# Performance work log

Hardware: AMD Instinct MI355X
Metric: run time of the kernel (lower is better)

The kernel has to match this reference:

```python
import jax, jax.numpy as jnp
import numpy as np

N_NODES = 100000
N_EDGES = 1600000
DIM = 128
EPS = 1e-12


def l2_normalize(x):
    # F.normalize(x, p=2, dim=1) with eps=1e-12
    n = jnp.linalg.norm(x, axis=1, keepdims=True)
    return x / jnp.maximum(n, EPS)


def poincare_logmap0(x):
    # logmap at origin, curvature c=1: artanh(||x||) * x / ||x||
    n = jnp.linalg.norm(x, axis=1, keepdims=True)
    n_safe = jnp.maximum(n, EPS)
    n_cl = jnp.clip(n_safe, EPS, 1.0 - 1e-5)
    return jnp.arctanh(n_cl) * x / n_safe


def poincare_expmap0(v):
    # expmap at origin, curvature c=1: tanh(||v||) * v / ||v||
    n = jnp.linalg.norm(v, axis=1, keepdims=True)
    n_safe = jnp.maximum(n, EPS)
    return jnp.tanh(n_safe) * v / n_safe


def mean_aggregate(x, src, dst, n_nodes):
    # DGL copy_u + mean: for each dst node, mean of src-node features over
    # incoming edges; nodes with zero in-degree get zeros.
    msg_sum = jax.ops.segment_sum(x[src], dst, num_segments=n_nodes)  # [N, D]
    deg = jax.ops.segment_sum(jnp.ones_like(dst, dtype=x.dtype), dst,
                              num_segments=n_nodes)  # [N]
    deg = deg[:, None]
    return jnp.where(deg > 0, msg_sum / jnp.maximum(deg, 1.0), 0.0)


def setup_inputs() -> dict:
    key = jax.random.key(0)
    ks = jax.random.split(key, 11)
    e_emb = jax.random.normal(ks[0], (N_NODES, DIM), dtype=jnp.float32)
    b_raw = jax.random.normal(ks[1], (N_NODES, DIM), dtype=jnp.float32)
    # project into open unit Poincare ball (max norm ~0.9)
    b_norm = jnp.linalg.norm(b_raw, axis=1, keepdims=True)
    b_emb = b_raw * (0.9 * jnp.tanh(b_norm) / jnp.maximum(b_norm, EPS))
    s_emb = jax.random.normal(ks[2], (N_NODES, DIM), dtype=jnp.float32)
    src = jax.random.randint(ks[3], (N_EDGES,), 0, N_NODES, dtype=jnp.int32)
    dst = jax.random.randint(ks[4], (N_EDGES,), 0, N_NODES, dtype=jnp.int32)
    scale = 1.0 / np.sqrt(DIM)
    W_e = jax.random.uniform(ks[5], (DIM, DIM), jnp.float32, -scale, scale)
    b_e = jax.random.uniform(ks[6], (DIM,), jnp.float32, -scale, scale)
    W_b = jax.random.uniform(ks[7], (DIM, DIM), jnp.float32, -scale, scale)
    b_b = jax.random.uniform(ks[8], (DIM,), jnp.float32, -scale, scale)
    W_s = jax.random.uniform(ks[9], (DIM, DIM), jnp.float32, -scale, scale)
    b_s = jax.random.uniform(ks[10], (DIM,), jnp.float32, -scale, scale)
    return {"e_emb": e_emb, "b_emb": b_emb, "s_emb": s_emb,
            "W_e": W_e, "b_e": b_e, "W_b": W_b, "b_b": b_b,
            "W_s": W_s, "b_s": b_s, "src": src, "dst": dst}


def reference(e_emb, b_emb, s_emb, W_e, b_e, W_b, b_b, W_s, b_s, src, dst):
    n = e_emb.shape[0]
    # Euclidean branch: aggregate -> linear -> LeakyReLU(0.2)
    e_neigh = mean_aggregate(e_emb, src, dst, n)
    e_lin = e_neigh @ W_e.T + b_e
    e_out = jnp.where(e_lin >= 0, e_lin, 0.2 * e_lin)
    # Poincare branch: logmap0 -> linear -> aggregate -> expmap0
    b_tan = poincare_logmap0(b_emb)
    b_tr = b_tan @ W_b.T + b_b
    b_neigh = mean_aggregate(b_tr, src, dst, n)
    b_out = poincare_expmap0(b_neigh)
    # Spherical branch: normalize -> linear -> aggregate -> normalize
    s_nrm = l2_normalize(s_emb)
    s_tr = s_nrm @ W_s.T + b_s
    s_neigh = mean_aggregate(s_tr, src, dst, n)
    s_out = l2_normalize(s_neigh)
    return (e_out, b_out, s_out)
```

## Files before the change

### kernel.cpp

```cpp
#include <hip/hip_runtime.h>
#include <math.h>

#define N_NODESC 100000
#define N_EDGESC 1600000
#define DIMC 128
#define EPSV 1e-12f

typedef __attribute__((ext_vector_type(8))) short short8;
typedef __attribute__((ext_vector_type(4))) float f32x4;
typedef __attribute__((ext_vector_type(2))) float f32x2;

__device__ inline unsigned bf16r(float f) {
    unsigned u = __float_as_uint(f);
    return (u + 0x7FFFu + ((u >> 16) & 1u)) >> 16;
}
__device__ inline unsigned pack2(float lo, float hi) {
    return bf16r(lo) | (bf16r(hi) << 16);
}
__device__ inline float unlo(unsigned u) { return __uint_as_float(u << 16); }
__device__ inline float unhi(unsigned u) { return __uint_as_float(u & 0xFFFF0000u); }

__device__ inline void bfsplit(float f, unsigned& h, unsigned& l) {
    h = bf16r(f);
    float fh = __uint_as_float(h << 16);
    l = bf16r(f - fh);
}

__global__ void pretransform_k(const float* __restrict__ e_emb,
                               const float* __restrict__ b_emb,
                               const float* __restrict__ s_emb,
                               const int* __restrict__ dst,
                               unsigned* __restrict__ tab,
                               int* __restrict__ deg) {
    {
        int e = blockIdx.x * 64 + threadIdx.x;
        if (threadIdx.x < 64 && e < N_EDGESC) atomicAdd(&deg[dst[e]], 1);
    }
    int wave = (blockIdx.x * blockDim.x + threadIdx.x) >> 6;
    int lane = threadIdx.x & 63;
    if (wave >= N_NODESC) return;
    f32x2 ev = __builtin_nontemporal_load((const f32x2*)(e_emb + (size_t)wave * DIMC) + lane);
    f32x2 bv = __builtin_nontemporal_load((const f32x2*)(b_emb + (size_t)wave * DIMC) + lane);
    f32x2 sv = __builtin_nontemporal_load((const f32x2*)(s_emb + (size_t)wave * DIMC) + lane);
    float bss = bv.x * bv.x + bv.y * bv.y;
    float sss = sv.x * sv.x + sv.y * sv.y;
    #pragma unroll
    for (int m = 1; m < 64; m <<= 1) {
        bss += __shfl_xor(bss, m, 64);
        sss += __shfl_xor(sss, m, 64);
    }
    float bn  = sqrtf(bss);
    float bns = fmaxf(bn, EPSV);
    float bcl = fminf(fmaxf(bns, EPSV), 1.0f - 1e-5f);
    float bsc = atanhf(bcl) / bns;
    float sn  = sqrtf(sss);
    float ssc = 1.0f / fmaxf(sn, EPSV);
    unsigned* p = tab + (size_t)wave * 192 + lane * 3;
    uint3 v;
    v.x = pack2(ev.x, ev.y);
    v.y = pack2(bv.x * bsc, bv.y * bsc);
    v.z = pack2(sv.x * ssc, sv.y * ssc);
    *(uint3*)p = v;
}

__global__ void scan1_k(const int* __restrict__ deg, int* __restrict__ scanned,
                        int* __restrict__ partials) {
    __shared__ int s[256];
    int t = threadIdx.x;
    int g = blockIdx.x * 256 + t;
    int v = (g < N_NODESC) ? deg[g] : 0;
    s[t] = v;
    __syncthreads();
    for (int off = 1; off < 256; off <<= 1) {
        int x = (t >= off) ? s[t - off] : 0;
        __syncthreads();
        s[t] += x;
        __syncthreads();
    }
    if (g < N_NODESC) scanned[g] = s[t];
    if (t == 255) partials[blockIdx.x] = s[255];
}

__global__ void scan2_k(const int* __restrict__ partials, int* __restrict__ blockoff, int nb) {
    __shared__ int s[512];
    int t = threadIdx.x;
    int v = (t < nb) ? partials[t] : 0;
    s[t] = v;
    __syncthreads();
    for (int off = 1; off < 512; off <<= 1) {
        int x = (t >= off) ? s[t - off] : 0;
        __syncthreads();
        s[t] += x;
        __syncthreads();
    }
    if (t < nb) blockoff[t] = s[t] - v;
}

__global__ void scan3_k(const int* __restrict__ scanned, const int* __restrict__ blockoff,
                        int* __restrict__ offs) {
    int g = blockIdx.x * 256 + threadIdx.x;
    if (g < N_NODESC) offs[g + 1] = scanned[g] + blockoff[blockIdx.x];
    if (g == 0) offs[0] = 0;
}

__global__ void fill_k(const int* __restrict__ src, const int* __restrict__ dst,
                       const int* __restrict__ offs, int* __restrict__ cursor,
                       int* __restrict__ esrc) {
    int e = blockIdx.x * 256 + threadIdx.x;
    if (e < N_EDGESC) {
        int d = __builtin_nontemporal_load(dst + e);
        int sv = __builtin_nontemporal_load(src + e);
        int pos = offs[d] + atomicAdd(&cursor[d], 1);
        esrc[pos] = sv;
    }
}

__global__ void aggregate_k(const unsigned* __restrict__ tab,
                            const int* __restrict__ offs,
                            const int* __restrict__ esrc,
                            float* __restrict__ out) {
    int wave = (blockIdx.x * blockDim.x + threadIdx.x) >> 6;
    int lane = threadIdx.x & 63;
    if (wave >= N_NODESC) return;
    int beg = offs[wave], end = offs[wave + 1];
    float ae0 = 0.f, ae1 = 0.f, ab0 = 0.f, ab1 = 0.f, as0 = 0.f, as1 = 0.f;
    int j = beg;
    int lo3 = lane * 3;
    for (; j + 1 < end; j += 2) {
        int s0 = esrc[j], s1 = esrc[j + 1];
        uint3 v0 = *(const uint3*)(tab + (size_t)s0 * 192 + lo3);
        uint3 v1 = *(const uint3*)(tab + (size_t)s1 * 192 + lo3);
        ae0 += unlo(v0.x); ae1 += unhi(v0.x);
        ab0 += unlo(v0.y); ab1 += unhi(v0.y);
        as0 += unlo(v0.z); as1 += unhi(v0.z);
        ae0 += unlo(v1.x); ae1 += unhi(v1.x);
        ab0 += unlo(v1.y); ab1 += unhi(v1.y);
        as0 += unlo(v1.z); as1 += unhi(v1.z);
    }
    if (j < end) {
        int s0 = esrc[j];
        uint3 v0 = *(const uint3*)(tab + (size_t)s0 * 192 + lo3);
        ae0 += unlo(v0.x); ae1 += unhi(v0.x);
        ab0 += unlo(v0.y); ab1 += unhi(v0.y);
        as0 += unlo(v0.z); as1 += unhi(v0.z);
    }
    int deg = end - beg;
    float inv = (deg > 0) ? 1.0f / (float)deg : 0.0f;
    ((float2*)(out + (size_t)wave * DIMC))[lane]                           = make_float2(ae0 * inv, ae1 * inv);
    ((float2*)(out + (size_t)(N_NODESC + wave) * DIMC))[lane]              = make_float2(ab0 * inv, ab1 * inv);
    ((float2*)(out + (size_t)(2 * (size_t)N_NODESC + wave) * DIMC))[lane]  = make_float2(as0 * inv, as1 * inv);
}

__global__ __launch_bounds__(256, 2) void gemm_mfma_k(
    float* __restrict__ out,
    const float* __restrict__ W_e, const float* __restrict__ b_e,
    const float* __restrict__ W_b, const float* __restrict__ b_b,
    const float* __restrict__ W_s, const float* __restrict__ b_s,
    const int* __restrict__ deg) {
    __shared__ unsigned short Wh[128][72];
    __shared__ unsigned short Wl[128][72];
    int c = blockIdx.y;
    const float* W    = (c == 0) ? W_e : (c == 1) ? W_b : W_s;
    const float* bias = (c == 0) ? b_e : (c == 1) ? b_b : b_s;
    float* A = out + (size_t)c * N_NODESC * DIMC;

    int tid = threadIdx.x;
    int wid = tid >> 6, lane = tid & 63;
    int m0 = blockIdx.x * 64;
    int arow = m0 + wid * 16 + (lane & 15);
    int kb = (lane >> 4) * 8;
    bool rowok = (arow < N_NODESC);
    const float* Ap = A + (size_t)arow * DIMC + kb;
    int colw = lane & 15;

    f32x4 acc[8] = {};

    for (int h = 0; h < 2; ++h) {
        short8 Ah[2], Al[2];
        #pragma unroll
        for (int ks = 0; ks < 2; ++ks) {
            float4 a0 = make_float4(0.f, 0.f, 0.f, 0.f);
            float4 a1 = a0;
            if (rowok) {
                a0 = *(const float4*)(Ap + h * 64 + ks * 32);
                a1 = *(const float4*)(Ap + h * 64 + ks * 32 + 4);
            }
            #define SPLIT8(val, idx) { unsigned hh, ll; bfsplit(val, hh, ll); \
                Ah[ks][idx] = (short)hh; Al[ks][idx] = (short)ll; }
            SPLIT8(a0.x, 0) SPLIT8(a0.y, 1) SPLIT8(a0.z, 2) SPLIT8(a0.w, 3)
            SPLIT8(a1.x, 4) SPLIT8(a1.y, 5) SPLIT8(a1.z, 6) SPLIT8(a1.w, 7)
            #undef SPLIT8
        }
        if (h) __syncthreads();
        #pragma unroll
        for (int r = 0; r < 8; ++r) {
            int flat = (r * 256 + tid) * 4;
            int n  = flat >> 6;
            int kk = flat & 63;
            float4 w4 = *(const float4*)(W + (size_t)n * DIMC + h * 64 + kk);
            unsigned h0, h1, h2, h3, l0, l1, l2, l3;
            bfsplit(w4.x, h0, l0); bfsplit(w4.y, h1, l1);
            bfsplit(w4.z, h2, l2); bfsplit(w4.w, h3, l3);
            *(uint2*)&Wh[n][kk] = make_uint2(h0 | (h1 << 16), h2 | (h3 << 16));
            *(uint2*)&Wl[n][kk] = make_uint2(l0 | (l1 << 16), l2 | (l3 << 16));
        }
        __syncthreads();
        #pragma unroll
        for (int n = 0; n < 8; ++n) {
            int col = n * 16 + colw;
            #pragma unroll
            for (int ks = 0; ks < 2; ++ks) {
                short8 wh = *(const short8*)&Wh[col][ks * 32 + kb];
                short8 wl = *(const short8*)&Wl[col][ks * 32 + kb];
                acc[n] = __builtin_amdgcn_mfma_f32_16x16x32_bf16(Ah[ks], wh, acc[n], 0, 0, 0);
                acc[n] = __builtin_amdgcn_mfma_f32_16x16x32_bf16(Al[ks], wh, acc[n], 0, 0, 0);
                acc[n] = __builtin_amdgcn_mfma_f32_16x16x32_bf16(Ah[ks], wl, acc[n], 0, 0, 0);
            }
        }
    }

    int r0 = m0 + wid * 16 + (lane >> 4) * 4;
    float bn[8];
    #pragma unroll
    for (int n = 0; n < 8; ++n) bn[n] = bias[n * 16 + colw];

    if (c == 0) {
        #pragma unroll
        for (int rg = 0; rg < 4; ++rg) {
            int row = r0 + rg;
            if (row >= N_NODESC) continue;
            float* Ar = A + (size_t)row * DIMC;
            #pragma unroll
            for (int n = 0; n < 8; ++n) {
                float z = acc[n][rg] + bn[n];
                float o = (z >= 0.f) ? z : 0.2f * z;
                __builtin_nontemporal_store(o, &Ar[n * 16 + colw]);
            }
        }
    } else {
        #pragma unroll
        for (int rg = 0; rg < 4; ++rg) {
            float z[8];
            float ss = 0.f;
            #pragma unroll
            for (int n = 0; n < 8; ++n) {
                z[n] = acc[n][rg] + bn[n];
                ss += z[n] * z[n];
            }
            ss += __shfl_xor(ss, 1, 64);
            ss += __shfl_xor(ss, 2, 64);
            ss += __shfl_xor(ss, 4, 64);
            ss += __shfl_xor(ss, 8, 64);
            float nrm = sqrtf(ss);
            float scale;
            if (c == 1) {
                float nsafe = fmaxf(nrm, EPSV);
                scale = tanhf(nsafe) / nsafe;
            } else {
                scale = 1.0f / fmaxf(nrm, EPSV);
            }
            int row = r0 + rg;
            if (row < N_NODESC) {
                if (deg[row] <= 0) scale = 0.0f;
                float* Ar = A + (size_t)row * DIMC;
                #pragma unroll
                for (int n = 0; n < 8; ++n)
                    __builtin_nontemporal_store(z[n] * scale, &Ar[n * 16 + colw]);
            }
        }
    }
}

extern "C" void kernel_launch(void* const* d_in, const int* in_sizes, int n_in,
                              void* d_out, int out_size, void* d_ws, size_t ws_size,
                              hipStream_t stream) {
    const float* e_emb = (const float*)d_in[0];
    const float* b_emb = (const float*)d_in[1];
    const float* s_emb = (const float*)d_in[2];
    const float* W_e   = (const float*)d_in[3];
    const float* b_e   = (const float*)d_in[4];
    const float* W_b   = (const float*)d_in[5];
    const float* b_b   = (const float*)d_in[6];
    const float* W_s   = (const float*)d_in[7];
    const float* b_s   = (const float*)d_in[8];
    const int*   src   = (const int*)d_in[9];
    const int*   dst   = (const int*)d_in[10];
    float* out = (float*)d_out;

    char* w = (char*)d_ws;
    unsigned* tab = (unsigned*)w; w += (size_t)N_NODESC * 192 * sizeof(unsigned);
    int* deg      = (int*)w;   w += (size_t)N_NODESC * sizeof(int);
    int* cursor   = (int*)w;   w += (size_t)N_NODESC * sizeof(int);
    int* scanned  = (int*)w;   w += (size_t)N_NODESC * sizeof(int);
    int* partials = (int*)w;   w += 512 * sizeof(int);
    int* blockoff = (int*)w;   w += 512 * sizeof(int);
    int* offs     = (int*)w;   w += (size_t)(N_NODESC + 1) * sizeof(int);
    w = (char*)(((uintptr_t)w + 255) & ~(uintptr_t)255);
    int* esrc     = (int*)w;   w += (size_t)N_EDGESC * sizeof(int);

    const int nbScan  = (N_NODESC + 255) / 256;
    const int nbEdge  = (N_EDGESC + 255) / 256;
    const int nbNode4 = (N_NODESC + 3) / 4;
    const int nbTile  = (N_NODESC + 63) / 64;

    hipMemsetAsync(deg, 0, (size_t)2 * N_NODESC * sizeof(int), stream);

    pretransform_k<<<nbNode4, 256, 0, stream>>>(e_emb, b_emb, s_emb, dst, tab, deg);
    scan1_k<<<nbScan, 256, 0, stream>>>(deg, scanned, partials);
    scan2_k<<<1, 512, 0, stream>>>(partials, blockoff, nbScan);
    scan3_k<<<nbScan, 256, 0, stream>>>(scanned, blockoff, offs);
    fill_k<<<nbEdge, 256, 0, stream>>>(src, dst, offs, cursor, esrc);
    aggregate_k<<<nbNode4, 256, 0, stream>>>(tab, offs, esrc, out);
    gemm_mfma_k<<<dim3(nbTile, 3), 256, 0, stream>>>(out, W_e, b_e, W_b, b_b, W_s, b_s, deg);
}
```

Baseline: 632.9 us.

## Split packed feature table into per-channel planes and aggregate each channel separately

The pretransform now writes the three bf16 branch features into three separate planar tables instead of one interleaved 12-byte-per-lane record. The aggregation kernel launches three times as many waves, one per (channel, node), each gathering a compact 256-byte row per edge. The aim is a smaller, contiguous gather footprint per channel and better cache locality. In exchange, the CSR offsets and edge source indices are read three times and each wave issues smaller loads.

```diff
diff --git a/kernel.cpp b/kernel.cpp
--- a/kernel.cpp
+++ b/kernel.cpp
@@ -55,12 +55,10 @@
     float bsc = atanhf(bcl) / bns;
     float sn  = sqrtf(sss);
     float ssc = 1.0f / fmaxf(sn, EPSV);
-    unsigned* p = tab + (size_t)wave * 192 + lane * 3;
-    uint3 v;
-    v.x = pack2(ev.x, ev.y);
-    v.y = pack2(bv.x * bsc, bv.y * bsc);
-    v.z = pack2(sv.x * ssc, sv.y * ssc);
-    *(uint3*)p = v;
+    size_t base = (size_t)wave * 64 + lane;
+    tab[base]                            = pack2(ev.x, ev.y);
+    tab[(size_t)N_NODESC * 64 + base]    = pack2(bv.x * bsc, bv.y * bsc);
+    tab[(size_t)N_NODESC * 128 + base]   = pack2(sv.x * ssc, sv.y * ssc);
 }
 
 __global__ void scan1_k(const int* __restrict__ deg, int* __restrict__ scanned,
@@ -119,36 +117,30 @@
                             const int* __restrict__ offs,
                             const int* __restrict__ esrc,
                             float* __restrict__ out) {
-    int wave = (blockIdx.x * blockDim.x + threadIdx.x) >> 6;
+    int gw = (blockIdx.x * blockDim.x + threadIdx.x) >> 6;
     int lane = threadIdx.x & 63;
-    if (wave >= N_NODESC) return;
-    int beg = offs[wave], end = offs[wave + 1];
-    float ae0 = 0.f, ae1 = 0.f, ab0 = 0.f, ab1 = 0.f, as0 = 0.f, as1 = 0.f;
+    int ch = gw / N_NODESC;
+    int node = gw - ch * N_NODESC;
+    if (ch >= 3) return;
+    const unsigned* tabc = tab + (size_t)ch * N_NODESC * 64;
+    int beg = offs[node], end = offs[node + 1];
+    float a0 = 0.f, a1 = 0.f;
     int j = beg;
-    int lo3 = lane * 3;
     for (; j + 1 < end; j += 2) {
         int s0 = esrc[j], s1 = esrc[j + 1];
-        uint3 v0 = *(const uint3*)(tab + (size_t)s0 * 192 + lo3);
-        uint3 v1 = *(const uint3*)(tab + (size_t)s1 * 192 + lo3);
-        ae0 += unlo(v0.x); ae1 += unhi(v0.x);
-        ab0 += unlo(v0.y); ab1 += unhi(v0.y);
-        as0 += unlo(v0.z); as1 += unhi(v0.z);
-        ae0 += unlo(v1.x); ae1 += unhi(v1.x);
-        ab0 += unlo(v1.y); ab1 += unhi(v1.y);
-        as0 += unlo(v1.z); as1 += unhi(v1.z);
+        unsigned v0 = tabc[(size_t)s0 * 64 + lane];
+        unsigned v1 = tabc[(size_t)s1 * 64 + lane];
+        a0 += unlo(v0); a1 += unhi(v0);
+        a0 += unlo(v1); a1 += unhi(v1);
     }
     if (j < end) {
         int s0 = esrc[j];
-        uint3 v0 = *(const uint3*)(tab + (size_t)s0 * 192 + lo3);
-        ae0 += unlo(v0.x); ae1 += unhi(v0.x);
-        ab0 += unlo(v0.y); ab1 += unhi(v0.y);
-        as0 += unlo(v0.z); as1 += unhi(v0.z);
+        unsigned v0 = tabc[(size_t)s0 * 64 + lane];
+        a0 += unlo(v0); a1 += unhi(v0);
     }
     int deg = end - beg;
     float inv = (deg > 0) ? 1.0f / (float)deg : 0.0f;
-    ((float2*)(out + (size_t)wave * DIMC))[lane]                           = make_float2(ae0 * inv, ae1 * inv);
-    ((float2*)(out + (size_t)(N_NODESC + wave) * DIMC))[lane]              = make_float2(ab0 * inv, ab1 * inv);
-    ((float2*)(out + (size_t)(2 * (size_t)N_NODESC + wave) * DIMC))[lane]  = make_float2(as0 * inv, as1 * inv);
+    ((float2*)(out + ((size_t)ch * N_NODESC + node) * DIMC))[lane] = make_float2(a0 * inv, a1 * inv);
 }
 
 __global__ __launch_bounds__(256, 2) void gemm_mfma_k(
@@ -310,6 +302,6 @@
     scan2_k<<<1, 512, 0, stream>>>(partials, blockoff, nbScan);
     scan3_k<<<nbScan, 256, 0, stream>>>(scanned, blockoff, offs);
     fill_k<<<nbEdge, 256, 0, stream>>>(src, dst, offs, cursor, esrc);
-    aggregate_k<<<nbNode4, 256, 0, stream>>>(tab, offs, esrc, out);
+    aggregate_k<<<nbNode4 * 3, 256, 0, stream>>>(tab, offs, esrc, out);
     gemm_mfma_k<<<dim3(nbTile, 3), 256, 0, stream>>>(out, W_e, b_e, W_b, b_b, W_s, b_s, deg);
 }
```

After: 729.9 us. 15.3% more time.

## Fuse mean aggregation with split-bf16 MFMA GEMM and epilogue per 16-row tile

Applied to the files above, without the earlier changes.

Merges the aggregation and GEMM kernels into one. Each block gathers neighbour means for 16 nodes into shared memory, then runs the three 128x128 linear layers with split-bf16 MFMA and applies the activation and normalization epilogues directly. This removes the fp32 intermediate round trip through global memory (about 150 MB written and read back). A small pre-kernel splits the weights into bf16 hi/lo once, so blocks read them from global/L2 instead of re-splitting them. The cost is fewer rows per block, so each block's weight fetch is amortized over less work, and the gather latency and MFMA phases are serialized within a block.

```diff
diff --git a/kernel.cpp b/kernel.cpp
--- a/kernel.cpp
+++ b/kernel.cpp
@@ -24,6 +24,22 @@
     h = bf16r(f);
     float fh = __uint_as_float(h << 16);
     l = bf16r(f - fh);
+}
+
+__global__ void wsplit_k(const float* __restrict__ W_e,
+                         const float* __restrict__ W_b,
+                         const float* __restrict__ W_s,
+                         unsigned short* __restrict__ whl) {
+    int idx = blockIdx.x * 256 + threadIdx.x;
+    if (idx >= 3 * 128 * 128) return;
+    int ch = idx >> 14;
+    int rem = idx & 16383;
+    const float* W = (ch == 0) ? W_e : (ch == 1) ? W_b : W_s;
+    float v = W[rem];
+    unsigned h, l;
+    bfsplit(v, h, l);
+    whl[(size_t)(ch * 2 + 0) * 16384 + rem] = (unsigned short)h;
+    whl[(size_t)(ch * 2 + 1) * 16384 + rem] = (unsigned short)l;
 }
 
 __global__ void pretransform_k(const float* __restrict__ e_emb,
@@ -115,157 +131,131 @@
     }
 }
 
-__global__ void aggregate_k(const unsigned* __restrict__ tab,
-                            const int* __restrict__ offs,
-                            const int* __restrict__ esrc,
-                            float* __restrict__ out) {
-    int wave = (blockIdx.x * blockDim.x + threadIdx.x) >> 6;
-    int lane = threadIdx.x & 63;
-    if (wave >= N_NODESC) return;
-    int beg = offs[wave], end = offs[wave + 1];
-    float ae0 = 0.f, ae1 = 0.f, ab0 = 0.f, ab1 = 0.f, as0 = 0.f, as1 = 0.f;
-    int j = beg;
-    int lo3 = lane * 3;
-    for (; j + 1 < end; j += 2) {
-        int s0 = esrc[j], s1 = esrc[j + 1];
-        uint3 v0 = *(const uint3*)(tab + (size_t)s0 * 192 + lo3);
-        uint3 v1 = *(const uint3*)(tab + (size_t)s1 * 192 + lo3);
-        ae0 += unlo(v0.x); ae1 += unhi(v0.x);
-        ab0 += unlo(v0.y); ab1 += unhi(v0.y);
-        as0 += unlo(v0.z); as1 += unhi(v0.z);
-        ae0 += unlo(v1.x); ae1 += unhi(v1.x);
-        ab0 += unlo(v1.y); ab1 += unhi(v1.y);
-        as0 += unlo(v1.z); as1 += unhi(v1.z);
-    }
-    if (j < end) {
-        int s0 = esrc[j];
-        uint3 v0 = *(const uint3*)(tab + (size_t)s0 * 192 + lo3);
-        ae0 += unlo(v0.x); ae1 += unhi(v0.x);
-        ab0 += unlo(v0.y); ab1 += unhi(v0.y);
-        as0 += unlo(v0.z); as1 += unhi(v0.z);
-    }
-    int deg = end - beg;
-    float inv = (deg > 0) ? 1.0f / (float)deg : 0.0f;
-    ((float2*)(out + (size_t)wave * DIMC))[lane]                           = make_float2(ae0 * inv, ae1 * inv);
-    ((float2*)(out + (size_t)(N_NODESC + wave) * DIMC))[lane]              = make_float2(ab0 * inv, ab1 * inv);
-    ((float2*)(out + (size_t)(2 * (size_t)N_NODESC + wave) * DIMC))[lane]  = make_float2(as0 * inv, as1 * inv);
-}
-
-__global__ __launch_bounds__(256, 2) void gemm_mfma_k(
-    float* __restrict__ out,
-    const float* __restrict__ W_e, const float* __restrict__ b_e,
-    const float* __restrict__ W_b, const float* __restrict__ b_b,
-    const float* __restrict__ W_s, const float* __restrict__ b_s,
-    const int* __restrict__ deg) {
-    __shared__ unsigned short Wh[128][72];
-    __shared__ unsigned short Wl[128][72];
-    int c = blockIdx.y;
-    const float* W    = (c == 0) ? W_e : (c == 1) ? W_b : W_s;
-    const float* bias = (c == 0) ? b_e : (c == 1) ? b_b : b_s;
-    float* A = out + (size_t)c * N_NODESC * DIMC;
+__global__ __launch_bounds__(256) void agg_gemm_k(
+    const unsigned* __restrict__ tab,
+    const int* __restrict__ offs,
+    const int* __restrict__ esrc,
+    const unsigned short* __restrict__ whl,
+    const float* __restrict__ b_e, const float* __restrict__ b_b,
+    const float* __restrict__ b_s,
+    float* __restrict__ out) {
+    __shared__ float As[3][16][132];
+    __shared__ float ssq[2][4][16];
+    __shared__ int   degs[16];
 
     int tid = threadIdx.x;
     int wid = tid >> 6, lane = tid & 63;
-    int m0 = blockIdx.x * 64;
-    int arow = m0 + wid * 16 + (lane & 15);
+    int base = blockIdx.x * 16;
+
+    int lo3 = lane * 3;
+    for (int t = 0; t < 4; ++t) {
+        int r = wid * 4 + t;
+        int node = base + r;
+        int beg = offs[node], end = offs[node + 1];
+        float ae0 = 0.f, ae1 = 0.f, ab0 = 0.f, ab1 = 0.f, as0 = 0.f, as1 = 0.f;
+        int j = beg;
+        for (; j + 1 < end; j += 2) {
+            int s0 = esrc[j], s1 = esrc[j + 1];
+            uint3 v0 = *(const uint3*)(tab + (size_t)s0 * 192 + lo3);
+            uint3 v1 = *(const uint3*)(tab + (size_t)s1 * 192 + lo3);
+            ae0 += unlo(v0.x); ae1 += unhi(v0.x);
+            ab0 += unlo(v0.y); ab1 += unhi(v0.y);
+            as0 += unlo(v0.z); as1 += unhi(v0.z);
+            ae0 += unlo(v1.x); ae1 += unhi(v1.x);
+            ab0 += unlo(v1.y); ab1 += unhi(v1.y);
+            as0 += unlo(v1.z); as1 += unhi(v1.z);
+        }
+        if (j < end) {
+            int s0 = esrc[j];
+            uint3 v0 = *(const uint3*)(tab + (size_t)s0 * 192 + lo3);
+            ae0 += unlo(v0.x); ae1 += unhi(v0.x);
+            ab0 += unlo(v0.y); ab1 += unhi(v0.y);
+            as0 += unlo(v0.z); as1 += unhi(v0.z);
+        }
+        int dg = end - beg;
+        float inv = (dg > 0) ? 1.0f / (float)dg : 0.0f;
+        ((float2*)&As[0][r][0])[lane] = make_float2(ae0 * inv, ae1 * inv);
+        ((float2*)&As[1][r][0])[lane] = make_float2(ab0 * inv, ab1 * inv);
+        ((float2*)&As[2][r][0])[lane] = make_float2(as0 * inv, as1 * inv);
+        if (lane == 0) degs[r] = dg;
+    }
+    __syncthreads();
+
+    int colw = lane & 15;
     int kb = (lane >> 4) * 8;
-    bool rowok = (arow < N_NODESC);
-    const float* Ap = A + (size_t)arow * DIMC + kb;
-    int colw = lane & 15;
-
-    f32x4 acc[8] = {};
-
-    for (int h = 0; h < 2; ++h) {
-        short8 Ah[2], Al[2];
+    int rowq = (lane >> 4) * 4;
+
+    for (int ch = 0; ch < 3; ++ch) {
+        f32x4 acc[2] = {};
+        const unsigned short* Wh = whl + (size_t)(ch * 2 + 0) * 16384;
+        const unsigned short* Wl = whl + (size_t)(ch * 2 + 1) * 16384;
         #pragma unroll
-        for (int ks = 0; ks < 2; ++ks) {
-            float4 a0 = make_float4(0.f, 0.f, 0.f, 0.f);
-            float4 a1 = a0;
-            if (rowok) {
-                a0 = *(const float4*)(Ap + h * 64 + ks * 32);
-                a1 = *(const float4*)(Ap + h * 64 + ks * 32 + 4);
-            }
-            #define SPLIT8(val, idx) { unsigned hh, ll; bfsplit(val, hh, ll); \
-                Ah[ks][idx] = (short)hh; Al[ks][idx] = (short)ll; }
-            SPLIT8(a0.x, 0) SPLIT8(a0.y, 1) SPLIT8(a0.z, 2) SPLIT8(a0.w, 3)
-            SPLIT8(a1.x, 4) SPLIT8(a1.y, 5) SPLIT8(a1.z, 6) SPLIT8(a1.w, 7)
-            #undef SPLIT8
+        for (int ks = 0; ks < 4; ++ks) {
+            short8 Ah, Al;
+            #pragma unroll
+            for (int jj = 0; jj < 8; ++jj) {
+                float a = As[ch][colw][ks * 32 + kb + jj];
+                unsigned hh, ll;
+                bfsplit(a, hh, ll);
+                Ah[jj] = (short)hh; Al[jj] = (short)ll;
+            }
+            #pragma unroll
+            for (int n = 0; n < 2; ++n) {
+                int col = wid * 32 + n * 16 + colw;
+                short8 wh = *(const short8*)(Wh + (size_t)col * 128 + ks * 32 + kb);
+                short8 wl = *(const short8*)(Wl + (size_t)col * 128 + ks * 32 + kb);
+                acc[n] = __builtin_amdgcn_mfma_f32_16x16x32_bf16(Ah, wh, acc[n], 0, 0, 0);
+                acc[n] = __builtin_amdgcn_mfma_f32_16x16x32_bf16(Al, wh, acc[n], 0, 0, 0);
+                acc[n] = __builtin_amdgcn_mfma_f32_16x16x32_bf16(Ah, wl, acc[n], 0, 0, 0);
+            }
         }
-        if (h) __syncthreads();
-        #pragma unroll
-        for (int r = 0; r < 8; ++r) {
-            int flat = (r * 256 + tid) * 4;
-            int n  = flat >> 6;
-            int kk = flat & 63;
-            float4 w4 = *(const float4*)(W + (size_t)n * DIMC + h * 64 + kk);
-            unsigned h0, h1, h2, h3, l0, l1, l2, l3;
-            bfsplit(w4.x, h0, l0); bfsplit(w4.y, h1, l1);
-            bfsplit(w4.z, h2, l2); bfsplit(w4.w, h3, l3);
-            *(uint2*)&Wh[n][kk] = make_uint2(h0 | (h1 << 16), h2 | (h3 << 16));
-            *(uint2*)&Wl[n][kk] = make_uint2(l0 | (l1 << 16), l2 | (l3 << 16));
-        }
-        __syncthreads();
-        #pragma unroll
-        for (int n = 0; n < 8; ++n) {
-            int col = n * 16 + colw;
-            #pragma unroll
-            for (int ks = 0; ks < 2; ++ks) {
-                short8 wh = *(const short8*)&Wh[col][ks * 32 + kb];
-                short8 wl = *(const short8*)&Wl[col][ks * 32 + kb];
-                acc[n] = __builtin_amdgcn_mfma_f32_16x16x32_bf16(Ah[ks], wh, acc[n], 0, 0, 0);
-                acc[n] = __builtin_amdgcn_mfma_f32_16x16x32_bf16(Al[ks], wh, acc[n], 0, 0, 0);
-                acc[n] = __builtin_amdgcn_mfma_f32_16x16x32_bf16(Ah[ks], wl, acc[n], 0, 0, 0);
-            }
-        }
-    }
-
-    int r0 = m0 + wid * 16 + (lane >> 4) * 4;
-    float bn[8];
-    #pragma unroll
-    for (int n = 0; n < 8; ++n) bn[n] = bias[n * 16 + colw];
-
-    if (c == 0) {
-        #pragma unroll
-        for (int rg = 0; rg < 4; ++rg) {
-            int row = r0 + rg;
-            if (row >= N_NODESC) continue;
-            float* Ar = A + (size_t)row * DIMC;
-            #pragma unroll
-            for (int n = 0; n < 8; ++n) {
-                float z = acc[n][rg] + bn[n];
-                float o = (z >= 0.f) ? z : 0.2f * z;
-                __builtin_nontemporal_store(o, &Ar[n * 16 + colw]);
-            }
-        }
-    } else {
-        #pragma unroll
-        for (int rg = 0; rg < 4; ++rg) {
-            float z[8];
-            float ss = 0.f;
-            #pragma unroll
-            for (int n = 0; n < 8; ++n) {
-                z[n] = acc[n][rg] + bn[n];
-                ss += z[n] * z[n];
-            }
-            ss += __shfl_xor(ss, 1, 64);
-            ss += __shfl_xor(ss, 2, 64);
-            ss += __shfl_xor(ss, 4, 64);
-            ss += __shfl_xor(ss, 8, 64);
-            float nrm = sqrtf(ss);
-            float scale;
-            if (c == 1) {
-                float nsafe = fmaxf(nrm, EPSV);
-                scale = tanhf(nsafe) / nsafe;
-            } else {
-                scale = 1.0f / fmaxf(nrm, EPSV);
-            }
-            int row = r0 + rg;
-            if (row < N_NODESC) {
-                if (deg[row] <= 0) scale = 0.0f;
-                float* Ar = A + (size_t)row * DIMC;
-                #pragma unroll
-                for (int n = 0; n < 8; ++n)
-                    __builtin_nontemporal_store(z[n] * scale, &Ar[n * 16 + colw]);
+        const float* bias = (ch == 0) ? b_e : (ch == 1) ? b_b : b_s;
+        float bn0 = bias[wid * 32 + colw];
+        float bn1 = bias[wid * 32 + 16 + colw];
+        float* O = out + (size_t)ch * N_NODESC * DIMC;
+
+        if (ch == 0) {
+            #pragma unroll
+            for (int rg = 0; rg < 4; ++rg) {
+                int row = base + rowq + rg;
+                float z0 = acc[0][rg] + bn0;
+                float z1 = acc[1][rg] + bn1;
+                float o0 = (z0 >= 0.f) ? z0 : 0.2f * z0;
+                float o1 = (z1 >= 0.f) ? z1 : 0.2f * z1;
+                __builtin_nontemporal_store(o0, &O[(size_t)row * DIMC + wid * 32 + colw]);
+                __builtin_nontemporal_store(o1, &O[(size_t)row * DIMC + wid * 32 + 16 + colw]);
+            }
+        } else {
+            float z0[4], z1[4];
+            #pragma unroll
+            for (int rg = 0; rg < 4; ++rg) {
+                z0[rg] = acc[0][rg] + bn0;
+                z1[rg] = acc[1][rg] + bn1;
+                float p = z0[rg] * z0[rg] + z1[rg] * z1[rg];
+                p += __shfl_xor(p, 1, 64);
+                p += __shfl_xor(p, 2, 64);
+                p += __shfl_xor(p, 4, 64);
+                p += __shfl_xor(p, 8, 64);
+                if (colw == 0) ssq[ch - 1][wid][rowq + rg] = p;
+            }
+            __syncthreads();
+            #pragma unroll
+            for (int rg = 0; rg < 4; ++rg) {
+                int r = rowq + rg;
+                float ss = ssq[ch - 1][0][r] + ssq[ch - 1][1][r]
+                         + ssq[ch - 1][2][r] + ssq[ch - 1][3][r];
+                float nrm = sqrtf(ss);
+                float scale;
+                if (ch == 1) {
+                    float nsafe = fmaxf(nrm, EPSV);
+                    scale = tanhf(nsafe) / nsafe;
+                } else {
+                    scale = 1.0f / fmaxf(nrm, EPSV);
+                }
+                if (degs[r] <= 0) scale = 0.0f;
+                int row = base + r;
+                __builtin_nontemporal_store(z0[rg] * scale, &O[(size_t)row * DIMC + wid * 32 + colw]);
+                __builtin_nontemporal_store(z1[rg] * scale, &O[(size_t)row * DIMC + wid * 32 + 16 + colw]);
             }
         }
     }
@@ -297,19 +287,21 @@
     int* offs     = (int*)w;   w += (size_t)(N_NODESC + 1) * sizeof(int);
     w = (char*)(((uintptr_t)w + 255) & ~(uintptr_t)255);
     int* esrc     = (int*)w;   w += (size_t)N_EDGESC * sizeof(int);
+    w = (char*)(((uintptr_t)w + 255) & ~(uintptr_t)255);
+    unsigned short* whl = (unsigned short*)w; w += (size_t)3 * 2 * 128 * 128 * sizeof(unsigned short);
 
     const int nbScan  = (N_NODESC + 255) / 256;
     const int nbEdge  = (N_EDGESC + 255) / 256;
     const int nbNode4 = (N_NODESC + 3) / 4;
-    const int nbTile  = (N_NODESC + 63) / 64;
+    const int nbTile16 = N_NODESC / 16;
 
     hipMemsetAsync(deg, 0, (size_t)2 * N_NODESC * sizeof(int), stream);
 
+    wsplit_k<<<192, 256, 0, stream>>>(W_e, W_b, W_s, whl);
     pretransform_k<<<nbNode4, 256, 0, stream>>>(e_emb, b_emb, s_emb, dst, tab, deg);
     scan1_k<<<nbScan, 256, 0, stream>>>(deg, scanned, partials);
     scan2_k<<<1, 512, 0, stream>>>(partials, blockoff, nbScan);
     scan3_k<<<nbScan, 256, 0, stream>>>(scanned, blockoff, offs);
     fill_k<<<nbEdge, 256, 0, stream>>>(src, dst, offs, cursor, esrc);
-    aggregate_k<<<nbNode4, 256, 0, stream>>>(tab, offs, esrc, out);
-    gemm_mfma_k<<<dim3(nbTile, 3), 256, 0, stream>>>(out, W_e, b_e, W_b, b_b, W_s, b_s, deg);
-}
+    agg_gemm_k<<<nbTile16, 256, 0, stream>>>(tab, offs, esrc, whl, b_e, b_b, b_s, out);
+}
```

Result: slower. 669.3 us (+5.8%).
